# Performance work log

Hardware: AMD Instinct MI355X
Metric: run time of the kernel (lower is better)

## Reference

```python
import jax, jax.numpy as jnp
import numpy as np

HEAD_DIM = 256
SCALE = HEAD_DIM ** (-0.5)


def setup_inputs() -> dict:
    key = jax.random.key(0)
    ks = jax.random.split(key, 6)
    B, H, Lq, Lp, D = 8, 32, 16, 4096, HEAD_DIM
    Q = jax.random.normal(ks[0], (B, H, Lq, D), dtype=jnp.float32)
    K_prior = jax.random.normal(ks[1], (B, H, Lp, D), dtype=jnp.float32)
    V_prior = jax.random.normal(ks[2], (B, H, Lp, D), dtype=jnp.float32)
    K_active = jax.random.normal(ks[3], (B, H, Lq, D), dtype=jnp.float32)
    V_active = jax.random.normal(ks[4], (B, H, Lq, D), dtype=jnp.float32)
    prior_mask = jax.random.randint(ks[5], (B, H, Lq, Lp), 0, 2).astype(jnp.bool_)
    return {"Q": Q, "K_prior": K_prior, "V_prior": V_prior,
            "K_active": K_active, "V_active": V_active, "prior_mask": prior_mask}


def manual_softmax(prior_scores, active_scores):
    # Cross-block softmax merge: shared row max and shared denominator.
    max_score = jnp.maximum(jnp.max(prior_scores, axis=-1, keepdims=True),
                            jnp.max(active_scores, axis=-1, keepdims=True))
    exp_prior = jnp.exp(prior_scores - max_score)
    exp_active = jnp.exp(active_scores - max_score)
    denom = (jnp.sum(exp_prior, axis=-1, keepdims=True)
             + jnp.sum(exp_active, axis=-1, keepdims=True))
    return exp_prior / denom, exp_active / denom


def reference(Q, K_prior, V_prior, K_active, V_active, prior_mask):
    # scores: [B, H, Lq, Lkv]
    prior_scores = jnp.einsum('bhqd,bhkd->bhqk', Q, K_prior) * SCALE
    prior_scores = jnp.where(prior_mask, prior_scores,
                             jnp.finfo(prior_scores.dtype).min)
    active_scores = jnp.einsum('bhqd,bhkd->bhqk', Q, K_active) * SCALE
    softmax_prior, softmax_active = manual_softmax(prior_scores, active_scores)
    softmax_prior = softmax_prior.astype(Q.dtype)
    softmax_active = softmax_active.astype(Q.dtype)
    attn_prior = jnp.einsum('bhqk,bhkd->bhqd', softmax_prior, V_prior)
    attn_active = jnp.einsum('bhqk,bhkd->bhqd', softmax_active, V_active)
    return attn_prior + attn_active
```

## Files before the change

kernel.cpp:

```cpp
#include <hip/hip_runtime.h>
#include <hip/hip_bf16.h>

#define LQ 16
#define DD 256
#define LP 4096
#define NBH 256

typedef __attribute__((ext_vector_type(8))) short bf16x8;
typedef __attribute__((ext_vector_type(4))) float f32x4;

static constexpr float QSC = 0.0625f * 1.44269504088896340736f;
static constexpr float NEGBIG = -1e30f;
static constexpr float MINIT  = -1e4f;

__device__ inline unsigned cvt2(float a, float b) {
  unsigned r;
  asm("v_cvt_pk_bf16_f32 %0, %1, %2" : "=v"(r) : "v"(a), "v"(b));
  return r;
}

union FragU { unsigned u[4]; bf16x8 v; };

__device__ inline bf16x8 pack8(float a0,float a1,float a2,float a3,
                               float a4,float a5,float a6,float a7){
  FragU x;
  x.u[0]=cvt2(a0,a1); x.u[1]=cvt2(a2,a3); x.u[2]=cvt2(a4,a5); x.u[3]=cvt2(a6,a7);
  return x.v;
}

template<bool ACTIVE>
__device__ inline void chunk_body(const float* __restrict__ kb_bh,
                                  const float* __restrict__ vb_bh,
                                  const unsigned char* __restrict__ m8_bh,
                                  const int* __restrict__ m32_bh,
                                  bool mbool, int k0, int l15, int g, int dh,
                                  const bf16x8 (&qf)[8],
                                  f32x4 (&acc)[8], float& m, float& l)
{
  f32x4 sc0 = {0.f,0.f,0.f,0.f}, sc1 = {0.f,0.f,0.f,0.f};
  {
    const int r0 = ACTIVE ? l15 : (k0 + l15);
    const float* kr0 = kb_bh + (size_t)r0 * DD + 8*g;
    #pragma unroll
    for (int s = 0; s < 8; ++s) {
      float4 a = *(const float4*)(kr0 + 32*s);
      float4 b = *(const float4*)(kr0 + 32*s + 4);
      bf16x8 kf = pack8(a.x,a.y,a.z,a.w,b.x,b.y,b.z,b.w);
      sc0 = __builtin_amdgcn_mfma_f32_16x16x32_bf16(kf, qf[s], sc0, 0,0,0);
    }
  }
  if (!ACTIVE) {
    const float* kr1 = kb_bh + (size_t)(k0 + 16 + l15) * DD + 8*g;
    #pragma unroll
    for (int s = 0; s < 8; ++s) {
      float4 a = *(const float4*)(kr1 + 32*s);
      float4 b = *(const float4*)(kr1 + 32*s + 4);
      bf16x8 kf = pack8(a.x,a.y,a.z,a.w,b.x,b.y,b.z,b.w);
      sc1 = __builtin_amdgcn_mfma_f32_16x16x32_bf16(kf, qf[s], sc1, 0,0,0);
    }
  }

  int vo[8];
  #pragma unroll
  for (int j = 0; j < 8; ++j) {
    const int kv = 4*g + (j&3) + 16*(j>>2);
    vo[j] = (ACTIVE ? kv : (k0 + kv)) * DD + dh*128 + l15;
  }

  bf16x8 vfr[8];
  #pragma unroll
  for (int t = 0; t < 8; ++t) {
    float v0 = vb_bh[vo[0]+16*t], v1 = vb_bh[vo[1]+16*t],
          v2 = vb_bh[vo[2]+16*t], v3 = vb_bh[vo[3]+16*t];
    float v4=0.f, v5=0.f, v6=0.f, v7=0.f;
    if (!ACTIVE) { v4 = vb_bh[vo[4]+16*t]; v5 = vb_bh[vo[5]+16*t];
                   v6 = vb_bh[vo[6]+16*t]; v7 = vb_bh[vo[7]+16*t]; }
    vfr[t] = pack8(v0,v1,v2,v3,v4,v5,v6,v7);
  }

  float s8[8];
  if (!ACTIVE) {
    const int ka0 = k0 + 4*g, ka1 = k0 + 16 + 4*g;
    if (mbool) {
      unsigned w0 = *(const unsigned*)(m8_bh + (size_t)l15*LP + ka0);
      unsigned w1 = *(const unsigned*)(m8_bh + (size_t)l15*LP + ka1);
      #pragma unroll
      for (int j = 0; j < 4; ++j) {
        s8[j]   = ((w0>>(8*j))&0xFFu) ? sc0[j] : NEGBIG;
        s8[4+j] = ((w1>>(8*j))&0xFFu) ? sc1[j] : NEGBIG;
      }
    } else {
      int4 w0 = *(const int4*)(m32_bh + (size_t)l15*LP + ka0);
      int4 w1 = *(const int4*)(m32_bh + (size_t)l15*LP + ka1);
      s8[0]=w0.x?sc0[0]:NEGBIG; s8[1]=w0.y?sc0[1]:NEGBIG;
      s8[2]=w0.z?sc0[2]:NEGBIG; s8[3]=w0.w?sc0[3]:NEGBIG;
      s8[4]=w1.x?sc1[0]:NEGBIG; s8[5]=w1.y?sc1[1]:NEGBIG;
      s8[6]=w1.z?sc1[2]:NEGBIG; s8[7]=w1.w?sc1[3]:NEGBIG;
    }
  } else {
    #pragma unroll
    for (int j = 0; j < 4; ++j) { s8[j] = sc0[j]; s8[4+j] = NEGBIG; }
  }

  float mx = fmaxf(fmaxf(fmaxf(s8[0],s8[1]),fmaxf(s8[2],s8[3])),
                   fmaxf(fmaxf(s8[4],s8[5]),fmaxf(s8[6],s8[7])));
  mx = fmaxf(mx, __shfl_xor(mx,16));
  mx = fmaxf(mx, __shfl_xor(mx,32));
  const float mn = fmaxf(m, mx);
  const float f = __builtin_amdgcn_exp2f(m - mn);
  float p[8], ps = 0.f;
  #pragma unroll
  for (int j = 0; j < 8; ++j){ p[j] = __builtin_amdgcn_exp2f(s8[j]-mn); ps += p[j]; }
  ps += __shfl_xor(ps,16);
  ps += __shfl_xor(ps,32);
  l = l * f + ps;
  m = mn;
  #pragma unroll
  for (int t = 0; t < 8; ++t){ acc[t][0]*=f; acc[t][1]*=f; acc[t][2]*=f; acc[t][3]*=f; }

  bf16x8 pf = pack8(p[0],p[1],p[2],p[3],p[4],p[5],p[6],p[7]);

  #pragma unroll
  for (int t = 0; t < 8; ++t) {
    acc[t] = __builtin_amdgcn_mfma_f32_16x16x32_bf16(vfr[t], pf, acc[t], 0,0,0);
  }
}

__global__ __launch_bounds__(256, 4)
void attn_main(const float* __restrict__ Q, const float* __restrict__ Kp,
               const float* __restrict__ Vp, const float* __restrict__ Ka,
               const float* __restrict__ Va, const void* __restrict__ mask,
               float* __restrict__ out, float* __restrict__ dn)
{
  const int tid = threadIdx.x;
  const int lane = tid & 63;
  const int wid = tid >> 6;
  const int pair = wid >> 1, dh = wid & 1;
  const int bh = blockIdx.x >> 2;
  const int pg = (blockIdx.x & 3) * 2 + pair;
  const int l15 = lane & 15, g = lane >> 4;

  const unsigned char* m8all = (const unsigned char*)mask;
  unsigned probe = 0;
  for (int i = lane; i < 256; i += 64) probe |= m8all[4*i+1];
  const bool mbool = (__any(probe != 0) != 0);

  const float* qb = Q + ((size_t)bh*LQ + l15)*DD + 8*g;
  bf16x8 qf[8];
  #pragma unroll
  for (int s = 0; s < 8; ++s) {
    float4 a = *(const float4*)(qb + 32*s);
    float4 b = *(const float4*)(qb + 32*s + 4);
    qf[s] = pack8(a.x*QSC,a.y*QSC,a.z*QSC,a.w*QSC,
                  b.x*QSC,b.y*QSC,b.z*QSC,b.w*QSC);
  }

  f32x4 acc[8];
  #pragma unroll
  for (int t = 0; t < 8; ++t) acc[t] = (f32x4){0.f,0.f,0.f,0.f};
  float m = MINIT, l = 0.f;

  const float* kb_bh = Kp + (size_t)bh*LP*DD;
  const float* vb_bh = Vp + (size_t)bh*LP*DD;
  const unsigned char* m8_bh = m8all + (size_t)bh*LQ*LP;
  const int* m32_bh = (const int*)mask + (size_t)bh*LQ*LP;

  const int kbase = pg * 512;
  for (int c = 0; c < 16; ++c)
    chunk_body<false>(kb_bh, vb_bh, m8_bh, m32_bh, mbool,
                      kbase + 32*c, l15, g, dh, qf, acc, m, l);

  if (pg == 0)
    chunk_body<true>(Ka + (size_t)bh*LQ*DD, Va + (size_t)bh*LQ*DD,
                     nullptr, nullptr, mbool, 0, l15, g, dh, qf, acc, m, l);

  const float w = __builtin_amdgcn_exp2f(m);
  float* ob = out + ((size_t)bh*LQ + l15)*DD + dh*128 + 4*g;
  #pragma unroll
  for (int t = 0; t < 8; ++t) {
    atomicAdd(ob + 16*t + 0, w*acc[t][0]);
    atomicAdd(ob + 16*t + 1, w*acc[t][1]);
    atomicAdd(ob + 16*t + 2, w*acc[t][2]);
    atomicAdd(ob + 16*t + 3, w*acc[t][3]);
  }
  if (dh == 0 && g == 0)
    atomicAdd(dn + bh*LQ + l15, w*l);
}

__global__ void attn_norm(float* __restrict__ out, const float* __restrict__ dn)
{
  const int e = blockIdx.x * 256 + threadIdx.x;
  out[e] = out[e] / dn[e >> 8];
}

extern "C" void kernel_launch(void* const* d_in, const int* in_sizes, int n_in,
                              void* d_out, int out_size, void* d_ws, size_t ws_size,
                              hipStream_t stream) {
  const float* Q  = (const float*)d_in[0];
  const float* Kp = (const float*)d_in[1];
  const float* Vp = (const float*)d_in[2];
  const float* Ka = (const float*)d_in[3];
  const float* Va = (const float*)d_in[4];
  const void* mask = d_in[5];
  float* out = (float*)d_out;
  float* dn  = (float*)d_ws;

  hipMemsetAsync(out, 0, (size_t)out_size * sizeof(float), stream);
  hipMemsetAsync(dn, 0, NBH * LQ * sizeof(float), stream);
  attn_main<<<NBH*4, 256, 0, stream>>>(Q, Kp, Vp, Ka, Va, mask, out, dn);
  attn_norm<<<(NBH*LQ*DD)/256, 256, 0, stream>>>(out, dn);
}
```

Measured before the change: 546.2 us.

## Split QK score computation across the wave pair and exchange via LDS

Previously each of the two waves in a pair (dh=0/1) computed the full 32-key QK^T scores redundantly, each loading both 16-row K tiles. Now each wave computes one 16-key half, and the halves are swapped through a double-buffered shared memory array with a __syncthreads per chunk. This halves K global loads and QK MFMAs per wave. In exchange it adds a block-wide barrier every chunk, which may stall waves and cut latency hiding. Mask loads are hoisted before the K loads, and the active-block path is inlined.

```diff
diff --git a/kernel.cpp b/kernel.cpp
--- a/kernel.cpp
+++ b/kernel.cpp
@@ -28,103 +28,6 @@
   return x.v;
 }
 
-template<bool ACTIVE>
-__device__ inline void chunk_body(const float* __restrict__ kb_bh,
-                                  const float* __restrict__ vb_bh,
-                                  const unsigned char* __restrict__ m8_bh,
-                                  const int* __restrict__ m32_bh,
-                                  bool mbool, int k0, int l15, int g, int dh,
-                                  const bf16x8 (&qf)[8],
-                                  f32x4 (&acc)[8], float& m, float& l)
-{
-  f32x4 sc0 = {0.f,0.f,0.f,0.f}, sc1 = {0.f,0.f,0.f,0.f};
-  {
-    const int r0 = ACTIVE ? l15 : (k0 + l15);
-    const float* kr0 = kb_bh + (size_t)r0 * DD + 8*g;
-    #pragma unroll
-    for (int s = 0; s < 8; ++s) {
-      float4 a = *(const float4*)(kr0 + 32*s);
-      float4 b = *(const float4*)(kr0 + 32*s + 4);
-      bf16x8 kf = pack8(a.x,a.y,a.z,a.w,b.x,b.y,b.z,b.w);
-      sc0 = __builtin_amdgcn_mfma_f32_16x16x32_bf16(kf, qf[s], sc0, 0,0,0);
-    }
-  }
-  if (!ACTIVE) {
-    const float* kr1 = kb_bh + (size_t)(k0 + 16 + l15) * DD + 8*g;
-    #pragma unroll
-    for (int s = 0; s < 8; ++s) {
-      float4 a = *(const float4*)(kr1 + 32*s);
-      float4 b = *(const float4*)(kr1 + 32*s + 4);
-      bf16x8 kf = pack8(a.x,a.y,a.z,a.w,b.x,b.y,b.z,b.w);
-      sc1 = __builtin_amdgcn_mfma_f32_16x16x32_bf16(kf, qf[s], sc1, 0,0,0);
-    }
-  }
-
-  int vo[8];
-  #pragma unroll
-  for (int j = 0; j < 8; ++j) {
-    const int kv = 4*g + (j&3) + 16*(j>>2);
-    vo[j] = (ACTIVE ? kv : (k0 + kv)) * DD + dh*128 + l15;
-  }
-
-  bf16x8 vfr[8];
-  #pragma unroll
-  for (int t = 0; t < 8; ++t) {
-    float v0 = vb_bh[vo[0]+16*t], v1 = vb_bh[vo[1]+16*t],
-          v2 = vb_bh[vo[2]+16*t], v3 = vb_bh[vo[3]+16*t];
-    float v4=0.f, v5=0.f, v6=0.f, v7=0.f;
-    if (!ACTIVE) { v4 = vb_bh[vo[4]+16*t]; v5 = vb_bh[vo[5]+16*t];
-                   v6 = vb_bh[vo[6]+16*t]; v7 = vb_bh[vo[7]+16*t]; }
-    vfr[t] = pack8(v0,v1,v2,v3,v4,v5,v6,v7);
-  }
-
-  float s8[8];
-  if (!ACTIVE) {
-    const int ka0 = k0 + 4*g, ka1 = k0 + 16 + 4*g;
-    if (mbool) {
-      unsigned w0 = *(const unsigned*)(m8_bh + (size_t)l15*LP + ka0);
-      unsigned w1 = *(const unsigned*)(m8_bh + (size_t)l15*LP + ka1);
-      #pragma unroll
-      for (int j = 0; j < 4; ++j) {
-        s8[j]   = ((w0>>(8*j))&0xFFu) ? sc0[j] : NEGBIG;
-        s8[4+j] = ((w1>>(8*j))&0xFFu) ? sc1[j] : NEGBIG;
-      }
-    } else {
-      int4 w0 = *(const int4*)(m32_bh + (size_t)l15*LP + ka0);
-      int4 w1 = *(const int4*)(m32_bh + (size_t)l15*LP + ka1);
-      s8[0]=w0.x?sc0[0]:NEGBIG; s8[1]=w0.y?sc0[1]:NEGBIG;
-      s8[2]=w0.z?sc0[2]:NEGBIG; s8[3]=w0.w?sc0[3]:NEGBIG;
-      s8[4]=w1.x?sc1[0]:NEGBIG; s8[5]=w1.y?sc1[1]:NEGBIG;
-      s8[6]=w1.z?sc1[2]:NEGBIG; s8[7]=w1.w?sc1[3]:NEGBIG;
-    }
-  } else {
-    #pragma unroll
-    for (int j = 0; j < 4; ++j) { s8[j] = sc0[j]; s8[4+j] = NEGBIG; }
-  }
-
-  float mx = fmaxf(fmaxf(fmaxf(s8[0],s8[1]),fmaxf(s8[2],s8[3])),
-                   fmaxf(fmaxf(s8[4],s8[5]),fmaxf(s8[6],s8[7])));
-  mx = fmaxf(mx, __shfl_xor(mx,16));
-  mx = fmaxf(mx, __shfl_xor(mx,32));
-  const float mn = fmaxf(m, mx);
-  const float f = __builtin_amdgcn_exp2f(m - mn);
-  float p[8], ps = 0.f;
-  #pragma unroll
-  for (int j = 0; j < 8; ++j){ p[j] = __builtin_amdgcn_exp2f(s8[j]-mn); ps += p[j]; }
-  ps += __shfl_xor(ps,16);
-  ps += __shfl_xor(ps,32);
-  l = l * f + ps;
-  m = mn;
-  #pragma unroll
-  for (int t = 0; t < 8; ++t){ acc[t][0]*=f; acc[t][1]*=f; acc[t][2]*=f; acc[t][3]*=f; }
-
-  bf16x8 pf = pack8(p[0],p[1],p[2],p[3],p[4],p[5],p[6],p[7]);
-
-  #pragma unroll
-  for (int t = 0; t < 8; ++t) {
-    acc[t] = __builtin_amdgcn_mfma_f32_16x16x32_bf16(vfr[t], pf, acc[t], 0,0,0);
-  }
-}
 
 __global__ __launch_bounds__(256, 4)
 void attn_main(const float* __restrict__ Q, const float* __restrict__ Kp,
@@ -132,6 +35,8 @@
                const float* __restrict__ Va, const void* __restrict__ mask,
                float* __restrict__ out, float* __restrict__ dn)
 {
+  __shared__ __align__(16) float xch[2][2][2][64][4];
+
   const int tid = threadIdx.x;
   const int lane = tid & 63;
   const int wid = tid >> 6;
@@ -166,13 +71,137 @@
   const int* m32_bh = (const int*)mask + (size_t)bh*LQ*LP;
 
   const int kbase = pg * 512;
-  for (int c = 0; c < 16; ++c)
-    chunk_body<false>(kb_bh, vb_bh, m8_bh, m32_bh, mbool,
-                      kbase + 32*c, l15, g, dh, qf, acc, m, l);
-
-  if (pg == 0)
-    chunk_body<true>(Ka + (size_t)bh*LQ*DD, Va + (size_t)bh*LQ*DD,
-                     nullptr, nullptr, mbool, 0, l15, g, dh, qf, acc, m, l);
+
+  for (int c = 0; c < 16; ++c) {
+    const int k0 = kbase + 32*c;
+
+    unsigned mw0 = 0xFFFFFFFFu, mw1 = 0xFFFFFFFFu;
+    int4 mi0, mi1;
+    {
+      const int ka0 = k0 + 4*g, ka1 = k0 + 16 + 4*g;
+      if (mbool) {
+        mw0 = *(const unsigned*)(m8_bh + (size_t)l15*LP + ka0);
+        mw1 = *(const unsigned*)(m8_bh + (size_t)l15*LP + ka1);
+      } else {
+        mi0 = *(const int4*)(m32_bh + (size_t)l15*LP + ka0);
+        mi1 = *(const int4*)(m32_bh + (size_t)l15*LP + ka1);
+      }
+    }
+
+    f32x4 sco = {0.f,0.f,0.f,0.f};
+    {
+      const float* kr = kb_bh + (size_t)(k0 + 16*dh + l15) * DD + 8*g;
+      #pragma unroll
+      for (int s = 0; s < 8; ++s) {
+        float4 a = *(const float4*)(kr + 32*s);
+        float4 b = *(const float4*)(kr + 32*s + 4);
+        bf16x8 kf = pack8(a.x,a.y,a.z,a.w,b.x,b.y,b.z,b.w);
+        sco = __builtin_amdgcn_mfma_f32_16x16x32_bf16(kf, qf[s], sco, 0,0,0);
+      }
+    }
+
+    const int par = c & 1;
+    *(f32x4*)&xch[par][pair][dh][lane][0] = sco;
+    __syncthreads();
+
+    int vo[8];
+    #pragma unroll
+    for (int j = 0; j < 8; ++j) {
+      const int kv = 4*g + (j&3) + 16*(j>>2);
+      vo[j] = (k0 + kv) * DD + dh*128 + l15;
+    }
+    bf16x8 vfr[8];
+    #pragma unroll
+    for (int t = 0; t < 8; ++t) {
+      float v0 = vb_bh[vo[0]+16*t], v1 = vb_bh[vo[1]+16*t],
+            v2 = vb_bh[vo[2]+16*t], v3 = vb_bh[vo[3]+16*t];
+      float v4 = vb_bh[vo[4]+16*t], v5 = vb_bh[vo[5]+16*t],
+            v6 = vb_bh[vo[6]+16*t], v7 = vb_bh[vo[7]+16*t];
+      vfr[t] = pack8(v0,v1,v2,v3,v4,v5,v6,v7);
+    }
+
+    f32x4 oth = *(const f32x4*)&xch[par][pair][dh^1][lane][0];
+    const f32x4 lo = dh ? oth : sco;
+    const f32x4 hi = dh ? sco : oth;
+
+    float s8[8];
+    if (mbool) {
+      #pragma unroll
+      for (int j = 0; j < 4; ++j) {
+        s8[j]   = ((mw0>>(8*j))&0xFFu) ? lo[j] : NEGBIG;
+        s8[4+j] = ((mw1>>(8*j))&0xFFu) ? hi[j] : NEGBIG;
+      }
+    } else {
+      s8[0]=mi0.x?lo[0]:NEGBIG; s8[1]=mi0.y?lo[1]:NEGBIG;
+      s8[2]=mi0.z?lo[2]:NEGBIG; s8[3]=mi0.w?lo[3]:NEGBIG;
+      s8[4]=mi1.x?hi[0]:NEGBIG; s8[5]=mi1.y?hi[1]:NEGBIG;
+      s8[6]=mi1.z?hi[2]:NEGBIG; s8[7]=mi1.w?hi[3]:NEGBIG;
+    }
+
+    float mx = fmaxf(fmaxf(fmaxf(s8[0],s8[1]),fmaxf(s8[2],s8[3])),
+                     fmaxf(fmaxf(s8[4],s8[5]),fmaxf(s8[6],s8[7])));
+    mx = fmaxf(mx, __shfl_xor(mx,16));
+    mx = fmaxf(mx, __shfl_xor(mx,32));
+    const float mn = fmaxf(m, mx);
+    const float f = __builtin_amdgcn_exp2f(m - mn);
+    float p[8], ps = 0.f;
+    #pragma unroll
+    for (int j = 0; j < 8; ++j){ p[j] = __builtin_amdgcn_exp2f(s8[j]-mn); ps += p[j]; }
+    ps += __shfl_xor(ps,16);
+    ps += __shfl_xor(ps,32);
+    l = l * f + ps;
+    m = mn;
+    #pragma unroll
+    for (int t = 0; t < 8; ++t){ acc[t][0]*=f; acc[t][1]*=f; acc[t][2]*=f; acc[t][3]*=f; }
+
+    bf16x8 pf = pack8(p[0],p[1],p[2],p[3],p[4],p[5],p[6],p[7]);
+
+    #pragma unroll
+    for (int t = 0; t < 8; ++t)
+      acc[t] = __builtin_amdgcn_mfma_f32_16x16x32_bf16(vfr[t], pf, acc[t], 0,0,0);
+  }
+
+  if (pg == 0) {
+    const float* ka_bh = Ka + (size_t)bh*LQ*DD;
+    const float* va_bh = Va + (size_t)bh*LQ*DD;
+    f32x4 sc0 = {0.f,0.f,0.f,0.f};
+    const float* kr0 = ka_bh + (size_t)l15*DD + 8*g;
+    #pragma unroll
+    for (int s = 0; s < 8; ++s) {
+      float4 a = *(const float4*)(kr0 + 32*s);
+      float4 b = *(const float4*)(kr0 + 32*s + 4);
+      bf16x8 kf = pack8(a.x,a.y,a.z,a.w,b.x,b.y,b.z,b.w);
+      sc0 = __builtin_amdgcn_mfma_f32_16x16x32_bf16(kf, qf[s], sc0, 0,0,0);
+    }
+    float s8[8];
+    #pragma unroll
+    for (int j = 0; j < 4; ++j) { s8[j] = sc0[j]; s8[4+j] = NEGBIG; }
+
+    float mx = fmaxf(fmaxf(s8[0],s8[1]),fmaxf(s8[2],s8[3]));
+    mx = fmaxf(mx, __shfl_xor(mx,16));
+    mx = fmaxf(mx, __shfl_xor(mx,32));
+    const float mn = fmaxf(m, mx);
+    const float f = __builtin_amdgcn_exp2f(m - mn);
+    float p[8], ps = 0.f;
+    #pragma unroll
+    for (int j = 0; j < 8; ++j){ p[j] = __builtin_amdgcn_exp2f(s8[j]-mn); ps += p[j]; }
+    ps += __shfl_xor(ps,16);
+    ps += __shfl_xor(ps,32);
+    l = l * f + ps;
+    m = mn;
+    #pragma unroll
+    for (int t = 0; t < 8; ++t){ acc[t][0]*=f; acc[t][1]*=f; acc[t][2]*=f; acc[t][3]*=f; }
+
+    bf16x8 pf = pack8(p[0],p[1],p[2],p[3],p[4],p[5],p[6],p[7]);
+    #pragma unroll
+    for (int t = 0; t < 8; ++t) {
+      const int col = dh*128 + 16*t + l15;
+      float v0 = va_bh[(4*g+0)*DD + col], v1 = va_bh[(4*g+1)*DD + col],
+            v2 = va_bh[(4*g+2)*DD + col], v3 = va_bh[(4*g+3)*DD + col];
+      bf16x8 vf = pack8(v0,v1,v2,v3,0.f,0.f,0.f,0.f);
+      acc[t] = __builtin_amdgcn_mfma_f32_16x16x32_bf16(vf, pf, acc[t], 0,0,0);
+    }
+  }
 
   const float w = __builtin_amdgcn_exp2f(m);
   float* ob = out + ((size_t)bh*LQ + l15)*DD + dh*128 + 4*g;
```

New measurement: 607.5 us. 1.11x slower.
